# Kernel optimization log

Hardware: AMD Instinct MI355X
Metric: run time of the kernel (lower is better)

## Reference

```python
import jax, jax.numpy as jnp
import numpy as np
from jax import lax

SIGMA = 1.0
TRUNCATE = 4.0  # skimage.filters.gaussian default


def _gauss_kernel(sigma, truncate=TRUNCATE):
    radius = int(truncate * sigma + 0.5)
    t = np.arange(-radius, radius + 1, dtype=np.float32)
    k = np.exp(-0.5 * (t / sigma) ** 2)
    k = k / k.sum()
    return jnp.asarray(k), radius


def setup_inputs() -> dict:
    key = jax.random.key(0)
    x = jax.random.uniform(key, (128, 1, 512, 512), dtype=jnp.float32)
    return {"x": x}


def _blur(x, sigma=SIGMA):
    # x: [B, 1, H, W] -> squeeze channel like the torch module, blur, return [B, H, W]
    k, r = _gauss_kernel(sigma)
    K = 2 * r + 1
    # 'nearest' boundary mode of skimage == edge padding
    xp = jnp.pad(x, ((0, 0), (0, 0), (r, r), (r, r)), mode="edge")
    kh = k.reshape(1, 1, K, 1).astype(x.dtype)  # vertical pass
    kw = k.reshape(1, 1, 1, K).astype(x.dtype)  # horizontal pass
    dn = lax.conv_dimension_numbers(xp.shape, kh.shape, ("NCHW", "OIHW", "NCHW"))
    y = lax.conv_general_dilated(xp, kh, (1, 1), "VALID", dimension_numbers=dn)
    y = lax.conv_general_dilated(y, kw, (1, 1), "VALID", dimension_numbers=dn)
    return y[:, 0]  # [B, H, W], matching x_i.squeeze() per-sample output


def reference(x):
    return _blur(x)
```

## Files before the change

kernel.cpp:

```cpp
#include <hip/hip_runtime.h>

namespace {

constexpr int R   = 4;
constexpr int TS  = 64;
constexpr int HS  = TS + 2 * R;
constexpr int LSTR = HS + 1;
constexpr int IMG_H = 512;
constexpr int IMG_W = 512;

__global__ __launch_bounds__(256)
void gauss_blur_kernel(const float* __restrict__ in, float* __restrict__ out) {
    const float KW[9] = {
        1.3383062e-4f, 4.4318616e-3f, 5.3990966e-2f, 2.4197144e-1f,
        3.9894347e-1f, 2.4197144e-1f, 5.3990966e-2f, 4.4318616e-3f,
        1.3383062e-4f};

    __shared__ float s_in[HS * LSTR];
    __shared__ float s_v [TS * LSTR];

    const int tid = threadIdx.x;
    const int b   = blockIdx.z;
    const int ty0 = blockIdx.y * TS;
    const int tx0 = blockIdx.x * TS;

    const float* __restrict__ inb = in + (size_t)b * IMG_H * IMG_W;

    for (int i = tid; i < HS * HS; i += 256) {
        int ly = i / HS;
        int lx = i - ly * HS;
        int gy = ty0 + ly - R;
        gy = gy < 0 ? 0 : (gy > IMG_H - 1 ? IMG_H - 1 : gy);
        int gx = tx0 + lx - R;
        gx = gx < 0 ? 0 : (gx > IMG_W - 1 ? IMG_W - 1 : gx);
        s_in[ly * LSTR + lx] = inb[gy * IMG_W + gx];
    }
    __syncthreads();

    for (int i = tid; i < TS * HS; i += 256) {
        int ly = i / HS;
        int lx = i - ly * HS;
        float acc = 0.f;
        #pragma unroll
        for (int t = 0; t < 9; ++t)
            acc = fmaf(KW[t], s_in[(ly + t) * LSTR + lx], acc);
        s_v[ly * LSTR + lx] = acc;
    }
    __syncthreads();

    float* __restrict__ outb = out + (size_t)b * IMG_H * IMG_W;
    for (int i = tid; i < TS * TS; i += 256) {
        int ly = i >> 6;
        int lx = i & (TS - 1);
        float acc = 0.f;
        #pragma unroll
        for (int t = 0; t < 9; ++t)
            acc = fmaf(KW[t], s_v[ly * LSTR + lx + t], acc);
        outb[(ty0 + ly) * IMG_W + (tx0 + lx)] = acc;
    }
}

}

extern "C" void kernel_launch(void* const* d_in, const int* in_sizes, int n_in,
                              void* d_out, int out_size, void* d_ws, size_t ws_size,
                              hipStream_t stream) {
    const float* x = (const float*)d_in[0];
    float* out = (float*)d_out;

    const int batch = in_sizes[0] / (IMG_H * IMG_W);

    dim3 grid(IMG_W / TS, IMG_H / TS, batch);
    gauss_blur_kernel<<<grid, 256, 0, stream>>>(x, out);
}
```

Before: 73.00 us.

## Vectorize blur with float4 global/LDS accesses and shrink tile height

```diff
diff --git a/kernel.cpp b/kernel.cpp
--- a/kernel.cpp
+++ b/kernel.cpp
@@ -2,12 +2,19 @@
 
 namespace {
 
-constexpr int R   = 4;
-constexpr int TS  = 64;
-constexpr int HS  = TS + 2 * R;
-constexpr int LSTR = HS + 1;
+constexpr int R     = 4;
+constexpr int TSX   = 64;
+constexpr int TSY   = 32;
+constexpr int HSX   = TSX + 2*R;
+constexpr int HSY   = TSY + 2*R;
+constexpr int VSTR  = 76;
+constexpr int NVX   = HSX / 4;
 constexpr int IMG_H = 512;
 constexpr int IMG_W = 512;
+
+__device__ __forceinline__ int clampi(int v, int lo, int hi) {
+    return v < lo ? lo : (v > hi ? hi : v);
+}
 
 __global__ __launch_bounds__(256)
 void gauss_blur_kernel(const float* __restrict__ in, float* __restrict__ out) {
@@ -16,47 +23,71 @@
         3.9894347e-1f, 2.4197144e-1f, 5.3990966e-2f, 4.4318616e-3f,
         1.3383062e-4f};
 
-    __shared__ float s_in[HS * LSTR];
-    __shared__ float s_v [TS * LSTR];
+    __shared__ float s_in[HSY * VSTR];
+    __shared__ float s_v [TSY * VSTR];
 
     const int tid = threadIdx.x;
     const int b   = blockIdx.z;
-    const int ty0 = blockIdx.y * TS;
-    const int tx0 = blockIdx.x * TS;
+    const int ty0 = blockIdx.y * TSY;
+    const int tx0 = blockIdx.x * TSX;
 
     const float* __restrict__ inb = in + (size_t)b * IMG_H * IMG_W;
 
-    for (int i = tid; i < HS * HS; i += 256) {
-        int ly = i / HS;
-        int lx = i - ly * HS;
-        int gy = ty0 + ly - R;
-        gy = gy < 0 ? 0 : (gy > IMG_H - 1 ? IMG_H - 1 : gy);
-        int gx = tx0 + lx - R;
-        gx = gx < 0 ? 0 : (gx > IMG_W - 1 ? IMG_W - 1 : gx);
-        s_in[ly * LSTR + lx] = inb[gy * IMG_W + gx];
+    for (int i = tid; i < HSY * NVX; i += 256) {
+        int ly = i / NVX;
+        int v  = i - ly * NVX;
+        int gy = clampi(ty0 + ly - R, 0, IMG_H - 1);
+        int gx = tx0 - R + 4 * v;
+        const float* rp = inb + gy * IMG_W;
+        float4 val;
+        if (gx >= 0 && gx <= IMG_W - 4) {
+            val = *reinterpret_cast<const float4*>(rp + gx);
+        } else {
+            val.x = rp[clampi(gx + 0, 0, IMG_W - 1)];
+            val.y = rp[clampi(gx + 1, 0, IMG_W - 1)];
+            val.z = rp[clampi(gx + 2, 0, IMG_W - 1)];
+            val.w = rp[clampi(gx + 3, 0, IMG_W - 1)];
+        }
+        *reinterpret_cast<float4*>(&s_in[ly * VSTR + 4 * v]) = val;
     }
     __syncthreads();
 
-    for (int i = tid; i < TS * HS; i += 256) {
-        int ly = i / HS;
-        int lx = i - ly * HS;
-        float acc = 0.f;
+    for (int i = tid; i < TSY * NVX; i += 256) {
+        int ly = i / NVX;
+        int v  = i - ly * NVX;
+        float4 acc = {0.f, 0.f, 0.f, 0.f};
         #pragma unroll
-        for (int t = 0; t < 9; ++t)
-            acc = fmaf(KW[t], s_in[(ly + t) * LSTR + lx], acc);
-        s_v[ly * LSTR + lx] = acc;
+        for (int t = 0; t < 9; ++t) {
+            float4 a = *reinterpret_cast<const float4*>(&s_in[(ly + t) * VSTR + 4 * v]);
+            acc.x = fmaf(KW[t], a.x, acc.x);
+            acc.y = fmaf(KW[t], a.y, acc.y);
+            acc.z = fmaf(KW[t], a.z, acc.z);
+            acc.w = fmaf(KW[t], a.w, acc.w);
+        }
+        *reinterpret_cast<float4*>(&s_v[ly * VSTR + 4 * v]) = acc;
     }
     __syncthreads();
 
     float* __restrict__ outb = out + (size_t)b * IMG_H * IMG_W;
-    for (int i = tid; i < TS * TS; i += 256) {
-        int ly = i >> 6;
-        int lx = i & (TS - 1);
-        float acc = 0.f;
+    for (int i = tid; i < TSY * (TSX / 4); i += 256) {
+        int ly = i >> 4;
+        int j  = i & 15;
+        const float* vp = &s_v[ly * VSTR + 4 * j];
+        float4 a = *reinterpret_cast<const float4*>(vp);
+        float4 bq = *reinterpret_cast<const float4*>(vp + 4);
+        float4 c = *reinterpret_cast<const float4*>(vp + 8);
+        float w[12] = {a.x, a.y, a.z, a.w, bq.x, bq.y, bq.z, bq.w, c.x, c.y, c.z, c.w};
+        float4 o;
+        float acc0 = 0.f, acc1 = 0.f, acc2 = 0.f, acc3 = 0.f;
         #pragma unroll
-        for (int t = 0; t < 9; ++t)
-            acc = fmaf(KW[t], s_v[ly * LSTR + lx + t], acc);
-        outb[(ty0 + ly) * IMG_W + (tx0 + lx)] = acc;
+        for (int t = 0; t < 9; ++t) {
+            acc0 = fmaf(KW[t], w[t + 0], acc0);
+            acc1 = fmaf(KW[t], w[t + 1], acc1);
+            acc2 = fmaf(KW[t], w[t + 2], acc2);
+            acc3 = fmaf(KW[t], w[t + 3], acc3);
+        }
+        o.x = acc0; o.y = acc1; o.z = acc2; o.w = acc3;
+        *reinterpret_cast<float4*>(&outb[(ty0 + ly) * IMG_W + tx0 + 4 * j]) = o;
     }
 }
 
@@ -70,6 +101,6 @@
 
     const int batch = in_sizes[0] / (IMG_H * IMG_W);
 
-    dim3 grid(IMG_W / TS, IMG_H / TS, batch);
+    dim3 grid(IMG_W / TSX, IMG_H / TSY, batch);
     gauss_blur_kernel<<<grid, 256, 0, stream>>>(x, out);
 }
```

Result: faster. 62.12 us (-14.9%).

## Replace shared-memory tiling with register-resident separable blur using float4 rows

Applied to the files above, without the earlier changes.

```diff
diff --git a/kernel.cpp b/kernel.cpp
--- a/kernel.cpp
+++ b/kernel.cpp
@@ -2,12 +2,14 @@
 
 namespace {
 
-constexpr int R   = 4;
-constexpr int TS  = 64;
-constexpr int HS  = TS + 2 * R;
-constexpr int LSTR = HS + 1;
-constexpr int IMG_H = 512;
-constexpr int IMG_W = 512;
+constexpr int IMG = 512;
+constexpr int PH  = 8;
+constexpr int BW_ = 256;
+constexpr int BH_ = 32;
+
+__device__ __forceinline__ int clampi(int v, int lo, int hi) {
+    return v < lo ? lo : (v > hi ? hi : v);
+}
 
 __global__ __launch_bounds__(256)
 void gauss_blur_kernel(const float* __restrict__ in, float* __restrict__ out) {
@@ -16,47 +18,72 @@
         3.9894347e-1f, 2.4197144e-1f, 5.3990966e-2f, 4.4318616e-3f,
         1.3383062e-4f};
 
-    __shared__ float s_in[HS * LSTR];
-    __shared__ float s_v [TS * LSTR];
+    const int tid  = threadIdx.x;
+    const int lane = tid & 63;
+    const int wave = tid >> 6;
+    const int b    = blockIdx.z;
+    const int x0   = blockIdx.x * BW_ + 4 * lane;
+    const int y0   = blockIdx.y * BH_ + wave * PH;
 
-    const int tid = threadIdx.x;
-    const int b   = blockIdx.z;
-    const int ty0 = blockIdx.y * TS;
-    const int tx0 = blockIdx.x * TS;
+    const float* __restrict__ inb = in + (size_t)b * IMG * IMG;
 
-    const float* __restrict__ inb = in + (size_t)b * IMG_H * IMG_W;
+    const bool edgeL = (x0 == 0);
+    const bool edgeR = (x0 + 4 == IMG);
 
-    for (int i = tid; i < HS * HS; i += 256) {
-        int ly = i / HS;
-        int lx = i - ly * HS;
-        int gy = ty0 + ly - R;
-        gy = gy < 0 ? 0 : (gy > IMG_H - 1 ? IMG_H - 1 : gy);
-        int gx = tx0 + lx - R;
-        gx = gx < 0 ? 0 : (gx > IMG_W - 1 ? IMG_W - 1 : gx);
-        s_in[ly * LSTR + lx] = inb[gy * IMG_W + gx];
+    float4 raw[3][3];
+
+    auto load_row = [&](int r, int slot) {
+        const int gy = clampi(y0 - 4 + r, 0, IMG - 1);
+        const float* rp = inb + (size_t)gy * IMG;
+        raw[slot][1] = *reinterpret_cast<const float4*>(rp + x0);
+        if (edgeL) { const float e = rp[0];       raw[slot][0] = make_float4(e, e, e, e); }
+        else       { raw[slot][0] = *reinterpret_cast<const float4*>(rp + x0 - 4); }
+        if (edgeR) { const float e = rp[IMG - 1]; raw[slot][2] = make_float4(e, e, e, e); }
+        else       { raw[slot][2] = *reinterpret_cast<const float4*>(rp + x0 + 4); }
+    };
+
+    load_row(0, 0);
+    load_row(1, 1);
+    load_row(2, 2);
+
+    float4 acc[PH] = {};
+
+    #pragma unroll
+    for (int r = 0; r < PH + 8; ++r) {
+        const int slot = r % 3;
+
+        const float w[12] = {
+            raw[slot][0].x, raw[slot][0].y, raw[slot][0].z, raw[slot][0].w,
+            raw[slot][1].x, raw[slot][1].y, raw[slot][1].z, raw[slot][1].w,
+            raw[slot][2].x, raw[slot][2].y, raw[slot][2].z, raw[slot][2].w};
+
+        if (r + 3 < PH + 8) load_row(r + 3, slot);
+
+        float h0 = 0.f, h1 = 0.f, h2 = 0.f, h3 = 0.f;
+        #pragma unroll
+        for (int t = 0; t < 9; ++t) {
+            h0 = fmaf(KW[t], w[t + 0], h0);
+            h1 = fmaf(KW[t], w[t + 1], h1);
+            h2 = fmaf(KW[t], w[t + 2], h2);
+            h3 = fmaf(KW[t], w[t + 3], h3);
+        }
+
+        #pragma unroll
+        for (int rr = 0; rr < PH; ++rr) {
+            const int k = r - rr;
+            if (k >= 0 && k < 9) {
+                acc[rr].x = fmaf(KW[k], h0, acc[rr].x);
+                acc[rr].y = fmaf(KW[k], h1, acc[rr].y);
+                acc[rr].z = fmaf(KW[k], h2, acc[rr].z);
+                acc[rr].w = fmaf(KW[k], h3, acc[rr].w);
+            }
+        }
     }
-    __syncthreads();
 
-    for (int i = tid; i < TS * HS; i += 256) {
-        int ly = i / HS;
-        int lx = i - ly * HS;
-        float acc = 0.f;
-        #pragma unroll
-        for (int t = 0; t < 9; ++t)
-            acc = fmaf(KW[t], s_in[(ly + t) * LSTR + lx], acc);
-        s_v[ly * LSTR + lx] = acc;
-    }
-    __syncthreads();
-
-    float* __restrict__ outb = out + (size_t)b * IMG_H * IMG_W;
-    for (int i = tid; i < TS * TS; i += 256) {
-        int ly = i >> 6;
-        int lx = i & (TS - 1);
-        float acc = 0.f;
-        #pragma unroll
-        for (int t = 0; t < 9; ++t)
-            acc = fmaf(KW[t], s_v[ly * LSTR + lx + t], acc);
-        outb[(ty0 + ly) * IMG_W + (tx0 + lx)] = acc;
+    float* __restrict__ outb = out + (size_t)b * IMG * IMG;
+    #pragma unroll
+    for (int rr = 0; rr < PH; ++rr) {
+        *reinterpret_cast<float4*>(&outb[(size_t)(y0 + rr) * IMG + x0]) = acc[rr];
     }
 }
 
@@ -68,8 +95,8 @@
     const float* x = (const float*)d_in[0];
     float* out = (float*)d_out;
 
-    const int batch = in_sizes[0] / (IMG_H * IMG_W);
+    const int batch = in_sizes[0] / (IMG * IMG);
 
-    dim3 grid(IMG_W / TS, IMG_H / TS, batch);
+    dim3 grid(IMG / BW_, IMG / BH_, batch);
     gauss_blur_kernel<<<grid, 256, 0, stream>>>(x, out);
 }
```

After: 143.1 us. 1.96x slower.
